# Performance work log

Hardware: AMD Instinct MI355X
Metric: run time of the kernel (lower is better)

Reference implementation:

```python
import jax, jax.numpy as jnp
import numpy as np
from jax.ops import segment_sum

NUM_NODES = 100000
HIDDEN = 128
NUM_LAYERS = 3
EDGES = 640000
BN_EPS = 1e-5


def setup_inputs() -> dict:
    key = jax.random.key(0)
    ks = jax.random.split(key, 6)
    edge_index = jax.random.randint(ks[0], (2, EDGES), 0, NUM_NODES, dtype=jnp.int32)
    # xavier-ish init for embedding (hidden-1 dims; last dim is log-degree feature)
    emb_weight = jax.random.normal(ks[1], (NUM_NODES, HIDDEN - 1), dtype=jnp.float32) * 0.02
    # GCNConv linear weights [L, in, out] and biases [L, out]
    Ws = jax.random.normal(ks[2], (NUM_LAYERS, HIDDEN, HIDDEN), dtype=jnp.float32) * (1.0 / np.sqrt(HIDDEN))
    bs = jnp.zeros((NUM_LAYERS, HIDDEN), dtype=jnp.float32)
    gammas = jnp.ones((NUM_LAYERS, HIDDEN), dtype=jnp.float32)
    betas = jnp.zeros((NUM_LAYERS, HIDDEN), dtype=jnp.float32)
    return {"emb_weight": emb_weight, "Ws": Ws, "bs": bs,
            "gammas": gammas, "betas": betas, "edge_index": edge_index}


def reference(emb_weight, Ws, bs, gammas, betas, edge_index):
    row, col = edge_index[0], edge_index[1]  # source, target
    N = emb_weight.shape[0]
    ones_e = jnp.ones(row.shape[0], dtype=emb_weight.dtype)

    # node_degree_features = log(out_degree + 1) (degree of edge_index[0])
    deg_src = segment_sum(ones_e, row, num_segments=N)
    x = jnp.concatenate([emb_weight, jnp.log(deg_src + 1.0)[:, None]], axis=1)  # [N, H]

    # GCN symmetric normalization (add_self_loops=False): deg over targets
    deg = segment_sum(ones_e, col, num_segments=N)
    dinv = jnp.where(deg > 0, jax.lax.rsqrt(jnp.maximum(deg, 1.0)), 0.0)
    norm = dinv[row] * dinv[col]  # [E]

    for i in range(Ws.shape[0]):
        x_prev = x
        h = x @ Ws[i]  # [N, H]
        # scatter-add of normalized messages: out[col] += norm * h[row]
        agg = segment_sum(norm[:, None] * h[row], col, num_segments=N) + bs[i]
        # BatchNorm1d (batch statistics, biased variance)
        mean = agg.mean(axis=0)
        var = agg.var(axis=0)
        x = gammas[i] * (agg - mean) * jax.lax.rsqrt(var + BN_EPS) + betas[i]
        x = jax.nn.relu(x)
        if i > 0:
            x = x + 0.5 * x_prev
    return x
```

## Files before the change

kernel.cpp:

```cpp
#include <hip/hip_runtime.h>
#include <hip/hip_bf16.h>
#include <math.h>

#define BN_EPS 1e-5f

typedef __attribute__((ext_vector_type(8))) short short8v;
typedef __attribute__((ext_vector_type(4))) float f32x4;
typedef __attribute__((ext_vector_type(2))) int int2v;
typedef __attribute__((ext_vector_type(4))) unsigned int uint4v;
typedef __attribute__((ext_vector_type(4))) float float4v;

__device__ inline float bf_lo(unsigned int p) { return __uint_as_float(p << 16); }
__device__ inline float bf_hi(unsigned int p) { return __uint_as_float(p & 0xffff0000u); }
__device__ inline unsigned int packbf(float a, float b) {
    unsigned short lo = __builtin_bit_cast(unsigned short, __float2bfloat16(a));
    unsigned short hi = __builtin_bit_cast(unsigned short, __float2bfloat16(b));
    return (unsigned int)lo | ((unsigned int)hi << 16);
}


__global__ __launch_bounds__(256) void deg_kernel(const int* __restrict__ row, const int* __restrict__ col,
                                                  float* __restrict__ deg_src, float* __restrict__ deg_dst, int E) {
    int e = blockIdx.x * 256 + threadIdx.x;
    if (e < E) {
        atomicAdd(&deg_src[row[e]], 1.0f);
        atomicAdd(&deg_dst[col[e]], 1.0f);
    }
}

__global__ __launch_bounds__(256) void dinv_cnt_kernel(float* __restrict__ deg_dst, int* __restrict__ cnt, int N) {
    int n = blockIdx.x * 256 + threadIdx.x;
    if (n < N) {
        float d = deg_dst[n];
        cnt[n] = (int)d;
        deg_dst[n] = (d > 0.0f) ? rsqrtf(d) : 0.0f;
    }
}

__global__ __launch_bounds__(256) void initx_kernel(const float* __restrict__ emb, const float* __restrict__ deg_src,
                                                    unsigned int* __restrict__ x, int N) {
    int idx = blockIdx.x * 256 + threadIdx.x;
    if (idx < N * 64) {
        int n = idx >> 6, p = idx & 63;
        float v0, v1;
        if (p < 63) {
            v0 = emb[(size_t)n * 127 + 2 * p];
            v1 = emb[(size_t)n * 127 + 2 * p + 1];
        } else {
            v0 = emb[(size_t)n * 127 + 126];
            v1 = logf(deg_src[n] + 1.0f);
        }
        x[idx] = packbf(v0, v1);
    }
}

__global__ __launch_bounds__(256) void wt_kernel(const float* __restrict__ Ws, __hip_bfloat16* __restrict__ Wt) {
    int idx = blockIdx.x * 256 + threadIdx.x;
    if (idx < 3 * 16384) {
        int l = idx >> 14, rem = idx & 16383, c = rem >> 7, k = rem & 127;
        Wt[idx] = __float2bfloat16(Ws[(l << 14) + (k << 7) + c]);
    }
}


__global__ __launch_bounds__(256) void scan_pass1(const int* __restrict__ cnt, int* __restrict__ blockSums,
                                                  int N, int PT) {
    __shared__ int lds[256];
    const int tid = threadIdx.x;
    const int start = (blockIdx.x * 256 + tid) * PT;
    int s = 0;
    for (int i = 0; i < PT; ++i) {
        int idx = start + i;
        if (idx < N) s += cnt[idx];
    }
    lds[tid] = s;
    __syncthreads();
    for (int d = 128; d > 0; d >>= 1) {
        if (tid < d) lds[tid] += lds[tid + d];
        __syncthreads();
    }
    if (tid == 0) blockSums[blockIdx.x] = lds[0];
}

__global__ __launch_bounds__(256) void scan_pass2(const int* __restrict__ blockSums, int* __restrict__ blockOffs) {
    __shared__ int lds[256];
    const int tid = threadIdx.x;
    int v = blockSums[tid];
    lds[tid] = v;
    __syncthreads();
    for (int d = 1; d < 256; d <<= 1) {
        int t = (tid >= d) ? lds[tid - d] : 0;
        __syncthreads();
        lds[tid] += t;
        __syncthreads();
    }
    blockOffs[tid] = lds[tid] - v;
}

__global__ __launch_bounds__(256) void scan_pass3(const int* __restrict__ cnt, const int* __restrict__ blockOffs,
                                                  int* __restrict__ off, int* __restrict__ cur,
                                                  int N, int PT, int E) {
    __shared__ int lds[256];
    const int tid = threadIdx.x;
    const int start = (blockIdx.x * 256 + tid) * PT;
    int s = 0;
    for (int i = 0; i < PT; ++i) {
        int idx = start + i;
        if (idx < N) s += cnt[idx];
    }
    lds[tid] = s;
    __syncthreads();
    for (int d = 1; d < 256; d <<= 1) {
        int t = (tid >= d) ? lds[tid - d] : 0;
        __syncthreads();
        lds[tid] += t;
        __syncthreads();
    }
    int prefix = blockOffs[blockIdx.x] + lds[tid] - s;
    for (int i = 0; i < PT; ++i) {
        int idx = start + i;
        if (idx < N) {
            off[idx] = prefix;
            cur[idx] = prefix;
            prefix += cnt[idx];
        }
    }
    if (blockIdx.x == 0 && tid == 0) off[N] = E;
}

__global__ __launch_bounds__(256) void fill_kernel(const int* __restrict__ row, const int* __restrict__ col,
                                                   const float* __restrict__ dinv, int* __restrict__ cur,
                                                   int2* __restrict__ meta, int E) {
    int e = blockIdx.x * 256 + threadIdx.x;
    if (e < E) {
        int r = row[e], t = col[e];
        int p = atomicAdd(&cur[t], 1);
        meta[p] = make_int2(r, __float_as_int(dinv[r] * dinv[t]));
    }
}


__global__ __launch_bounds__(256) void gemm_mfma(const __hip_bfloat16* __restrict__ X,
                                                 const __hip_bfloat16* __restrict__ Wt,
                                                 __hip_bfloat16* __restrict__ H, float* __restrict__ sums,
                                                 int nStripes, int N) {
    if (blockIdx.x == 0) sums[threadIdx.x] = 0.0f;

    const int lane = threadIdx.x & 63;
    const int wv = threadIdx.x >> 6;
    const int r = lane & 15;
    const int q = lane >> 4;
    const int ch = (blockIdx.x * 4 + wv) & 1;

    short8v bfrag[4][4];
#pragma unroll
    for (int ct = 0; ct < 4; ++ct)
#pragma unroll
        for (int kk = 0; kk < 4; ++kk)
            bfrag[ct][kk] = *(const short8v*)(Wt + ((ch * 64 + ct * 16 + r) << 7) + kk * 32 + q * 8);

    const int totalJobs = nStripes * 2;
    for (int job = blockIdx.x * 4 + wv; job < totalJobs; job += gridDim.x * 4) {
        const int s = job >> 1;
        const int arow = s * 16 + r;
        short8v a0 = {}, a1 = {}, a2 = {}, a3 = {};
        if (arow < N) {
            const __hip_bfloat16* xp = X + ((size_t)arow << 7) + q * 8;
            a0 = *(const short8v*)(xp);
            a1 = *(const short8v*)(xp + 32);
            a2 = *(const short8v*)(xp + 64);
            a3 = *(const short8v*)(xp + 96);
        }
        f32x4 acc[4];
#pragma unroll
        for (int ct = 0; ct < 4; ++ct) {
            f32x4 c = {0.f, 0.f, 0.f, 0.f};
            c = __builtin_amdgcn_mfma_f32_16x16x32_bf16(a0, bfrag[ct][0], c, 0, 0, 0);
            c = __builtin_amdgcn_mfma_f32_16x16x32_bf16(a1, bfrag[ct][1], c, 0, 0, 0);
            c = __builtin_amdgcn_mfma_f32_16x16x32_bf16(a2, bfrag[ct][2], c, 0, 0, 0);
            c = __builtin_amdgcn_mfma_f32_16x16x32_bf16(a3, bfrag[ct][3], c, 0, 0, 0);
            acc[ct] = c;
        }
#pragma unroll
        for (int g = 0; g < 4; ++g) {
            int grow = s * 16 + q * 4 + g;
            if (grow < N) {
                __hip_bfloat16* hp = H + ((size_t)grow << 7) + ch * 64 + r;
#pragma unroll
                for (int ct = 0; ct < 4; ++ct)
                    hp[ct * 16] = __float2bfloat16(acc[ct][g]);
            }
        }
    }
}


template <int MODE>
__global__ __launch_bounds__(256) void bn_gemm(const unsigned int* __restrict__ aggb, const float* __restrict__ sums,
                                               const float* __restrict__ gamma, const float* __restrict__ beta,
                                               const unsigned int* __restrict__ xprevb, unsigned int* __restrict__ xoutb,
                                               const __hip_bfloat16* __restrict__ Wt, __hip_bfloat16* __restrict__ H,
                                               float* __restrict__ sumsNext, int nStripes, int N, float invN) {
    if (blockIdx.x == 0) sumsNext[threadIdx.x] = 0.0f;

    const int lane = threadIdx.x & 63;
    const int wv = threadIdx.x >> 6;
    const int r = lane & 15;
    const int q = lane >> 4;
    const int ch = (blockIdx.x * 4 + wv) & 1;

    short8v bfrag[4][4];
#pragma unroll
    for (int ct = 0; ct < 4; ++ct)
#pragma unroll
        for (int kk = 0; kk < 4; ++kk)
            bfrag[ct][kk] = *(const short8v*)(Wt + ((ch * 64 + ct * 16 + r) << 7) + kk * 32 + q * 8);

    const int totalJobs = nStripes * 2;
    for (int job = blockIdx.x * 4 + wv; job < totalJobs; job += gridDim.x * 4) {
        const int s = job >> 1;
        const int arow = s * 16 + r;
        short8v a[4] = {{}, {}, {}, {}};
        if (arow < N) {
            const size_t rbase = ((size_t)arow << 6) + q * 4;
#pragma unroll
            for (int kk = 0; kk < 4; ++kk) {
                const int c0 = q * 8 + kk * 32;
                float su[8], sq[8], gm[8], bt[8];
                *(float4*)&su[0] = *(const float4*)&sums[c0];
                *(float4*)&su[4] = *(const float4*)&sums[c0 + 4];
                *(float4*)&sq[0] = *(const float4*)&sums[128 + c0];
                *(float4*)&sq[4] = *(const float4*)&sums[128 + c0 + 4];
                *(float4*)&gm[0] = *(const float4*)&gamma[c0];
                *(float4*)&gm[4] = *(const float4*)&gamma[c0 + 4];
                *(float4*)&bt[0] = *(const float4*)&beta[c0];
                *(float4*)&bt[4] = *(const float4*)&beta[c0 + 4];
                float sc[8], sh[8];
#pragma unroll
                for (int j = 0; j < 8; ++j) {
                    float m = su[j] * invN;
                    float v = sq[j] * invN - m * m;
                    float inv = rsqrtf(fmaxf(v, 0.0f) + BN_EPS);
                    sc[j] = gm[j] * inv;
                    sh[j] = bt[j] - m * sc[j];
                }
                uint4 av = *(const uint4*)(aggb + rbase + kk * 16);
                const unsigned int* au = (const unsigned int*)&av;
                float x[8];
#pragma unroll
                for (int j = 0; j < 4; ++j) {
                    x[2 * j]     = fmaxf(fmaf(bf_lo(au[j]), sc[2 * j],     sh[2 * j]),     0.f);
                    x[2 * j + 1] = fmaxf(fmaf(bf_hi(au[j]), sc[2 * j + 1], sh[2 * j + 1]), 0.f);
                }
                if (MODE == 1) {
                    uint4 xv = *(const uint4*)(xprevb + rbase + kk * 16);
                    const unsigned int* xu = (const unsigned int*)&xv;
#pragma unroll
                    for (int j = 0; j < 4; ++j) {
                        x[2 * j]     = fmaf(0.5f, bf_lo(xu[j]), x[2 * j]);
                        x[2 * j + 1] = fmaf(0.5f, bf_hi(xu[j]), x[2 * j + 1]);
                    }
                }
                uint4 pk;
                unsigned int* pku = (unsigned int*)&pk;
#pragma unroll
                for (int j = 0; j < 4; ++j) pku[j] = packbf(x[2 * j], x[2 * j + 1]);
                if (ch == 0) *(uint4*)(xoutb + rbase + kk * 16) = pk;
#pragma unroll
                for (int j = 0; j < 4; ++j) ((unsigned int*)&a[kk])[j] = pku[j];
            }
        }
        f32x4 acc[4];
#pragma unroll
        for (int ct = 0; ct < 4; ++ct) {
            f32x4 c = {0.f, 0.f, 0.f, 0.f};
            c = __builtin_amdgcn_mfma_f32_16x16x32_bf16(a[0], bfrag[ct][0], c, 0, 0, 0);
            c = __builtin_amdgcn_mfma_f32_16x16x32_bf16(a[1], bfrag[ct][1], c, 0, 0, 0);
            c = __builtin_amdgcn_mfma_f32_16x16x32_bf16(a[2], bfrag[ct][2], c, 0, 0, 0);
            c = __builtin_amdgcn_mfma_f32_16x16x32_bf16(a[3], bfrag[ct][3], c, 0, 0, 0);
            acc[ct] = c;
        }
#pragma unroll
        for (int g = 0; g < 4; ++g) {
            int grow = s * 16 + q * 4 + g;
            if (grow < N) {
                __hip_bfloat16* hp = H + ((size_t)grow << 7) + ch * 64 + r;
#pragma unroll
                for (int ct = 0; ct < 4; ++ct)
                    hp[ct * 16] = __float2bfloat16(acc[ct][g]);
            }
        }
    }
}


__global__ __launch_bounds__(256) void gather_kernel(const __hip_bfloat16* __restrict__ h,
                                                     const int* __restrict__ off, const int2* __restrict__ meta,
                                                     const float* __restrict__ bias,
                                                     unsigned int* __restrict__ aggb, float* __restrict__ sums, int N) {
    __shared__ float sm[2][4][128];
    const int tid = threadIdx.x;
    const int lane = tid & 63;
    const int w = tid >> 6;
    const int g = lane >> 4;
    const int s = lane & 15;

    float b8[8];
    *(float4*)&b8[0] = *(const float4*)&bias[s * 8];
    *(float4*)&b8[4] = *(const float4*)&bias[s * 8 + 4];

    float psum[8], psq[8];
#pragma unroll
    for (int j = 0; j < 8; ++j) { psum[j] = 0.f; psq[j] = 0.f; }

    for (int base = (blockIdx.x * 4 + w) * 2; base < N; base += gridDim.x * 8) {
        const int nA = __builtin_amdgcn_readfirstlane(base);
        const int hasB = (nA + 1 < N);
        const int sA = off[nA];
        const int eA = off[nA + 1];
        const int eB = hasB ? off[nA + 2] : eA;

        float accA[8], accB[8];
#pragma unroll
        for (int j = 0; j < 8; ++j) { accA[j] = 0.f; accB[j] = 0.f; }

        int iA = sA, iB = eA;
        while (iA < eA || iB < eB) {
            int i0A = iA + g, i1A = iA + 4 + g;
            int i0B = iB + g, i1B = iB + 4 + g;
            int idx0A = (i0A < eA) ? i0A : 0;
            int idx1A = (i1A < eA) ? i1A : 0;
            int idx0B = (i0B < eB) ? i0B : 0;
            int idx1B = (i1B < eB) ? i1B : 0;
            int2v m0A = __builtin_nontemporal_load((const int2v*)&meta[idx0A]);
            int2v m1A = __builtin_nontemporal_load((const int2v*)&meta[idx1A]);
            int2v m0B = __builtin_nontemporal_load((const int2v*)&meta[idx0B]);
            int2v m1B = __builtin_nontemporal_load((const int2v*)&meta[idx1B]);
            float w0A = (i0A < eA) ? __int_as_float(m0A[1]) : 0.f;
            float w1A = (i1A < eA) ? __int_as_float(m1A[1]) : 0.f;
            float w0B = (i0B < eB) ? __int_as_float(m0B[1]) : 0.f;
            float w1B = (i1B < eB) ? __int_as_float(m1B[1]) : 0.f;
            short8v h0A = *(const short8v*)(h + ((size_t)m0A[0] << 7) + s * 8);
            short8v h1A = *(const short8v*)(h + ((size_t)m1A[0] << 7) + s * 8);
            short8v h0B = *(const short8v*)(h + ((size_t)m0B[0] << 7) + s * 8);
            short8v h1B = *(const short8v*)(h + ((size_t)m1B[0] << 7) + s * 8);
#pragma unroll
            for (int j = 0; j < 4; ++j) {
                unsigned int u;
                u = ((const unsigned int*)&h0A)[j];
                accA[2 * j]     = fmaf(w0A, bf_lo(u), accA[2 * j]);
                accA[2 * j + 1] = fmaf(w0A, bf_hi(u), accA[2 * j + 1]);
                u = ((const unsigned int*)&h1A)[j];
                accA[2 * j]     = fmaf(w1A, bf_lo(u), accA[2 * j]);
                accA[2 * j + 1] = fmaf(w1A, bf_hi(u), accA[2 * j + 1]);
                u = ((const unsigned int*)&h0B)[j];
                accB[2 * j]     = fmaf(w0B, bf_lo(u), accB[2 * j]);
                accB[2 * j + 1] = fmaf(w0B, bf_hi(u), accB[2 * j + 1]);
                u = ((const unsigned int*)&h1B)[j];
                accB[2 * j]     = fmaf(w1B, bf_lo(u), accB[2 * j]);
                accB[2 * j + 1] = fmaf(w1B, bf_hi(u), accB[2 * j + 1]);
            }
            iA += 8; iB += 8;
        }
#pragma unroll
        for (int j = 0; j < 8; ++j) {
            accA[j] += __shfl_xor(accA[j], 16);
            accA[j] += __shfl_xor(accA[j], 32);
            accA[j] += b8[j];
            accB[j] += __shfl_xor(accB[j], 16);
            accB[j] += __shfl_xor(accB[j], 32);
            accB[j] += b8[j];
        }
        if (g == 0) {
            uint4v pk;
#pragma unroll
            for (int j = 0; j < 4; ++j) pk[j] = packbf(accA[2 * j], accA[2 * j + 1]);
            __builtin_nontemporal_store(pk, (uint4v*)(aggb + ((size_t)nA << 6) + s * 4));
#pragma unroll
            for (int j = 0; j < 8; ++j) {
                psum[j] += accA[j];
                psq[j] = fmaf(accA[j], accA[j], psq[j]);
            }
            if (hasB) {
#pragma unroll
                for (int j = 0; j < 8; ++j) {
                    psum[j] += accB[j];
                    psq[j] = fmaf(accB[j], accB[j], psq[j]);
                }
            }
        } else if (g == 1 && hasB) {
            uint4v pk;
#pragma unroll
            for (int j = 0; j < 4; ++j) pk[j] = packbf(accB[2 * j], accB[2 * j + 1]);
            __builtin_nontemporal_store(pk, (uint4v*)(aggb + ((size_t)(nA + 1) << 6) + s * 4));
        }
    }
    if (g == 0) {
#pragma unroll
        for (int j = 0; j < 8; ++j) {
            sm[0][w][s * 8 + j] = psum[j];
            sm[1][w][s * 8 + j] = psq[j];
        }
    }
    __syncthreads();
    if (tid < 128) {
        atomicAdd(&sums[tid], sm[0][0][tid] + sm[0][1][tid] + sm[0][2][tid] + sm[0][3][tid]);
    } else {
        int c = tid - 128;
        atomicAdd(&sums[128 + c], sm[1][0][c] + sm[1][1][c] + sm[1][2][c] + sm[1][3][c]);
    }
}


__global__ __launch_bounds__(256) void bn_out(const unsigned int* __restrict__ aggb, const float* __restrict__ sums,
                                              const float* __restrict__ gamma, const float* __restrict__ beta,
                                              const uint4* __restrict__ xprev, float* __restrict__ xout,
                                              int NO, float invN) {
    int idx = blockIdx.x * 256 + threadIdx.x;
    if (idx >= NO) return;
    const int c0 = (idx & 15) * 8;

    float su[8], sq[8], gm[8], bt[8];
    *(float4*)&su[0] = *(const float4*)&sums[c0];
    *(float4*)&su[4] = *(const float4*)&sums[c0 + 4];
    *(float4*)&sq[0] = *(const float4*)&sums[128 + c0];
    *(float4*)&sq[4] = *(const float4*)&sums[128 + c0 + 4];
    *(float4*)&gm[0] = *(const float4*)&gamma[c0];
    *(float4*)&gm[4] = *(const float4*)&gamma[c0 + 4];
    *(float4*)&bt[0] = *(const float4*)&beta[c0];
    *(float4*)&bt[4] = *(const float4*)&beta[c0 + 4];

    float sc[8], sh[8];
#pragma unroll
    for (int j = 0; j < 8; ++j) {
        float m = su[j] * invN;
        float v = sq[j] * invN - m * m;
        float inv = rsqrtf(fmaxf(v, 0.0f) + BN_EPS);
        sc[j] = gm[j] * inv;
        sh[j] = bt[j] - m * sc[j];
    }

    uint4v av = __builtin_nontemporal_load((const uint4v*)(aggb + (size_t)idx * 4));
    float r[8];
#pragma unroll
    for (int j = 0; j < 4; ++j) {
        r[2 * j]     = fmaxf(fmaf(bf_lo(av[j]), sc[2 * j],     sh[2 * j]),     0.f);
        r[2 * j + 1] = fmaxf(fmaf(bf_hi(av[j]), sc[2 * j + 1], sh[2 * j + 1]), 0.f);
    }
    uint4 xv = xprev[idx];
    const unsigned int* xu = (const unsigned int*)&xv;
#pragma unroll
    for (int j = 0; j < 4; ++j) {
        r[2 * j]     = fmaf(0.5f, bf_lo(xu[j]), r[2 * j]);
        r[2 * j + 1] = fmaf(0.5f, bf_hi(xu[j]), r[2 * j + 1]);
    }
    float* op = xout + (size_t)idx * 8;
    float4v lo = {r[0], r[1], r[2], r[3]};
    float4v hi = {r[4], r[5], r[6], r[7]};
    __builtin_nontemporal_store(lo, (float4v*)op);
    __builtin_nontemporal_store(hi, (float4v*)(op + 4));
}


extern "C" void kernel_launch(void* const* d_in, const int* in_sizes, int n_in,
                              void* d_out, int out_size, void* d_ws, size_t ws_size,
                              hipStream_t stream) {
    const float* emb    = (const float*)d_in[0];
    const float* Ws     = (const float*)d_in[1];
    const float* bs     = (const float*)d_in[2];
    const float* gammas = (const float*)d_in[3];
    const float* betas  = (const float*)d_in[4];
    const int*   ei     = (const int*)d_in[5];

    const int N = in_sizes[0] / 127;
    const int E = in_sizes[5] / 2;
    const int* row = ei;
    const int* col = ei + E;
    float* out = (float*)d_out;

    const size_t NH = (size_t)N * 128;
    __hip_bfloat16* XA = (__hip_bfloat16*)d_ws;
    __hip_bfloat16* XB = XA + NH;
    unsigned int*  AGG = (unsigned int*)(XB + NH);
    int2*         meta = (int2*)(AGG + NH / 2);
    __hip_bfloat16* Wt = (__hip_bfloat16*)(meta + E);
    float* deg_src = (float*)(Wt + 3 * 16384);
    float* dinvb   = deg_src + N;
    float* sumsA   = dinvb + N;
    float* sumsB   = sumsA + 256;
    int*   cnt     = (int*)(sumsB + 256);
    int*   cur     = cnt + N;
    int*   blockSums = cur + N;
    int*   blockOffs = blockSums + 256;
    int*   off     = blockOffs + 256;

    __hip_bfloat16* H2 = (__hip_bfloat16*)out;

    const int NO = (int)(NH / 8);
    const int PT = (N + 65535) / 65536;
    const int nStripes = (N + 15) / 16;
    const float invN = 1.0f / (float)N;

    hipMemsetAsync(deg_src, 0, sizeof(float) * 2 * (size_t)N, stream);
    wt_kernel<<<(3 * 16384 + 255) / 256, 256, 0, stream>>>(Ws, Wt);
    deg_kernel<<<(E + 255) / 256, 256, 0, stream>>>(row, col, deg_src, dinvb, E);
    dinv_cnt_kernel<<<(N + 255) / 256, 256, 0, stream>>>(dinvb, cnt, N);
    initx_kernel<<<(N * 64 + 255) / 256, 256, 0, stream>>>(emb, deg_src, (unsigned int*)XA, N);
    scan_pass1<<<256, 256, 0, stream>>>(cnt, blockSums, N, PT);
    scan_pass2<<<1, 256, 0, stream>>>(blockSums, blockOffs);
    scan_pass3<<<256, 256, 0, stream>>>(cnt, blockOffs, off, cur, N, PT, E);
    fill_kernel<<<(E + 255) / 256, 256, 0, stream>>>(row, col, dinvb, cur, meta, E);

    gemm_mfma<<<1024, 256, 0, stream>>>(XA, Wt, XB, sumsA, nStripes, N);
    gather_kernel<<<2048, 256, 0, stream>>>(XB, off, meta, bs, AGG, sumsA, N);

    bn_gemm<0><<<1024, 256, 0, stream>>>(AGG, sumsA, gammas, betas, nullptr,
                                         (unsigned int*)XA, Wt + 16384, XB, sumsB, nStripes, N, invN);
    gather_kernel<<<2048, 256, 0, stream>>>(XB, off, meta, bs + 128, AGG, sumsB, N);

    bn_gemm<1><<<1024, 256, 0, stream>>>(AGG, sumsB, gammas + 128, betas + 128, (const unsigned int*)XA,
                                         (unsigned int*)XB, Wt + 2 * 16384, H2, sumsA, nStripes, N, invN);
    gather_kernel<<<2048, 256, 0, stream>>>(H2, off, meta, bs + 256, AGG, sumsA, N);

    bn_out<<<(NO + 255) / 256, 256, 0, stream>>>(AGG, sumsA, gammas + 256, betas + 256,
                                                 (const uint4*)XB, out, NO, invN);
}
```

Measured before the change: 496.3 us.

## Fold dinv kernel into fill, precompute BN scale in LDS, drop nontemporal ops

Removes the dinv_cnt kernel: the scan reads float degrees directly and fill_kernel computes rsqrt of both endpoint degrees inline. bn_gemm now computes the BatchNorm scale and shift once per block into shared memory instead of recomputing them from global sums in every inner iteration. Nontemporal loads and stores in the gather and bn_out kernels are replaced with ordinary vector accesses. Together these save one launch and some redundant arithmetic and global reads, at the cost of an extra rsqrt per edge in fill and a block-wide sync in bn_gemm. Dropping the nontemporal hints changes how the caches treat those accesses.

```diff
diff --git a/kernel.cpp b/kernel.cpp
--- a/kernel.cpp
+++ b/kernel.cpp
@@ -6,8 +6,6 @@
 
 typedef __attribute__((ext_vector_type(8))) short short8v;
 typedef __attribute__((ext_vector_type(4))) float f32x4;
-typedef __attribute__((ext_vector_type(2))) int int2v;
-typedef __attribute__((ext_vector_type(4))) unsigned int uint4v;
 typedef __attribute__((ext_vector_type(4))) float float4v;
 
 __device__ inline float bf_lo(unsigned int p) { return __uint_as_float(p << 16); }
@@ -25,15 +23,6 @@
     if (e < E) {
         atomicAdd(&deg_src[row[e]], 1.0f);
         atomicAdd(&deg_dst[col[e]], 1.0f);
-    }
-}
-
-__global__ __launch_bounds__(256) void dinv_cnt_kernel(float* __restrict__ deg_dst, int* __restrict__ cnt, int N) {
-    int n = blockIdx.x * 256 + threadIdx.x;
-    if (n < N) {
-        float d = deg_dst[n];
-        cnt[n] = (int)d;
-        deg_dst[n] = (d > 0.0f) ? rsqrtf(d) : 0.0f;
     }
 }
 
@@ -63,7 +52,7 @@
 }
 
 
-__global__ __launch_bounds__(256) void scan_pass1(const int* __restrict__ cnt, int* __restrict__ blockSums,
+__global__ __launch_bounds__(256) void scan_pass1(const float* __restrict__ deg, int* __restrict__ blockSums,
                                                   int N, int PT) {
     __shared__ int lds[256];
     const int tid = threadIdx.x;
@@ -71,7 +60,7 @@
     int s = 0;
     for (int i = 0; i < PT; ++i) {
         int idx = start + i;
-        if (idx < N) s += cnt[idx];
+        if (idx < N) s += (int)deg[idx];
     }
     lds[tid] = s;
     __syncthreads();
@@ -97,7 +86,7 @@
     blockOffs[tid] = lds[tid] - v;
 }
 
-__global__ __launch_bounds__(256) void scan_pass3(const int* __restrict__ cnt, const int* __restrict__ blockOffs,
+__global__ __launch_bounds__(256) void scan_pass3(const float* __restrict__ deg, const int* __restrict__ blockOffs,
                                                   int* __restrict__ off, int* __restrict__ cur,
                                                   int N, int PT, int E) {
     __shared__ int lds[256];
@@ -106,7 +95,7 @@
     int s = 0;
     for (int i = 0; i < PT; ++i) {
         int idx = start + i;
-        if (idx < N) s += cnt[idx];
+        if (idx < N) s += (int)deg[idx];
     }
     lds[tid] = s;
     __syncthreads();
@@ -122,20 +111,23 @@
         if (idx < N) {
             off[idx] = prefix;
             cur[idx] = prefix;
-            prefix += cnt[idx];
+            prefix += (int)deg[idx];
         }
     }
     if (blockIdx.x == 0 && tid == 0) off[N] = E;
 }
 
 __global__ __launch_bounds__(256) void fill_kernel(const int* __restrict__ row, const int* __restrict__ col,
-                                                   const float* __restrict__ dinv, int* __restrict__ cur,
+                                                   const float* __restrict__ deg_dst, int* __restrict__ cur,
                                                    int2* __restrict__ meta, int E) {
     int e = blockIdx.x * 256 + threadIdx.x;
     if (e < E) {
         int r = row[e], t = col[e];
         int p = atomicAdd(&cur[t], 1);
-        meta[p] = make_int2(r, __float_as_int(dinv[r] * dinv[t]));
+        float dr = deg_dst[r], dt = deg_dst[t];
+        float ir = (dr > 0.0f) ? rsqrtf(dr) : 0.0f;
+        float it = (dt > 0.0f) ? rsqrtf(dt) : 0.0f;
+        meta[p] = make_int2(r, __float_as_int(ir * it));
     }
 }
 
@@ -201,10 +193,21 @@
                                                const unsigned int* __restrict__ xprevb, unsigned int* __restrict__ xoutb,
                                                const __hip_bfloat16* __restrict__ Wt, __hip_bfloat16* __restrict__ H,
                                                float* __restrict__ sumsNext, int nStripes, int N, float invN) {
-    if (blockIdx.x == 0) sumsNext[threadIdx.x] = 0.0f;
-
-    const int lane = threadIdx.x & 63;
-    const int wv = threadIdx.x >> 6;
+    __shared__ float ssc[128], ssh[128];
+    const int tid = threadIdx.x;
+    if (blockIdx.x == 0) sumsNext[tid] = 0.0f;
+    if (tid < 128) {
+        float m = sums[tid] * invN;
+        float v = sums[128 + tid] * invN - m * m;
+        float inv = rsqrtf(fmaxf(v, 0.0f) + BN_EPS);
+        float sc = gamma[tid] * inv;
+        ssc[tid] = sc;
+        ssh[tid] = beta[tid] - m * sc;
+    }
+    __syncthreads();
+
+    const int lane = tid & 63;
+    const int wv = tid >> 6;
     const int r = lane & 15;
     const int q = lane >> 4;
     const int ch = (blockIdx.x * 4 + wv) & 1;
@@ -226,24 +229,11 @@
 #pragma unroll
             for (int kk = 0; kk < 4; ++kk) {
                 const int c0 = q * 8 + kk * 32;
-                float su[8], sq[8], gm[8], bt[8];
-                *(float4*)&su[0] = *(const float4*)&sums[c0];
-                *(float4*)&su[4] = *(const float4*)&sums[c0 + 4];
-                *(float4*)&sq[0] = *(const float4*)&sums[128 + c0];
-                *(float4*)&sq[4] = *(const float4*)&sums[128 + c0 + 4];
-                *(float4*)&gm[0] = *(const float4*)&gamma[c0];
-                *(float4*)&gm[4] = *(const float4*)&gamma[c0 + 4];
-                *(float4*)&bt[0] = *(const float4*)&beta[c0];
-                *(float4*)&bt[4] = *(const float4*)&beta[c0 + 4];
                 float sc[8], sh[8];
-#pragma unroll
-                for (int j = 0; j < 8; ++j) {
-                    float m = su[j] * invN;
-                    float v = sq[j] * invN - m * m;
-                    float inv = rsqrtf(fmaxf(v, 0.0f) + BN_EPS);
-                    sc[j] = gm[j] * inv;
-                    sh[j] = bt[j] - m * sc[j];
-                }
+                *(float4*)&sc[0] = *(const float4*)&ssc[c0];
+                *(float4*)&sc[4] = *(const float4*)&ssc[c0 + 4];
+                *(float4*)&sh[0] = *(const float4*)&ssh[c0];
+                *(float4*)&sh[4] = *(const float4*)&ssh[c0 + 4];
                 uint4 av = *(const uint4*)(aggb + rbase + kk * 16);
                 const unsigned int* au = (const unsigned int*)&av;
                 float x[8];
@@ -332,18 +322,16 @@
             int idx1A = (i1A < eA) ? i1A : 0;
             int idx0B = (i0B < eB) ? i0B : 0;
             int idx1B = (i1B < eB) ? i1B : 0;
-            int2v m0A = __builtin_nontemporal_load((const int2v*)&meta[idx0A]);
-            int2v m1A = __builtin_nontemporal_load((const int2v*)&meta[idx1A]);
-            int2v m0B = __builtin_nontemporal_load((const int2v*)&meta[idx0B]);
-            int2v m1B = __builtin_nontemporal_load((const int2v*)&meta[idx1B]);
-            float w0A = (i0A < eA) ? __int_as_float(m0A[1]) : 0.f;
-            float w1A = (i1A < eA) ? __int_as_float(m1A[1]) : 0.f;
-            float w0B = (i0B < eB) ? __int_as_float(m0B[1]) : 0.f;
-            float w1B = (i1B < eB) ? __int_as_float(m1B[1]) : 0.f;
-            short8v h0A = *(const short8v*)(h + ((size_t)m0A[0] << 7) + s * 8);
-            short8v h1A = *(const short8v*)(h + ((size_t)m1A[0] << 7) + s * 8);
-            short8v h0B = *(const short8v*)(h + ((size_t)m0B[0] << 7) + s * 8);
-            short8v h1B = *(const short8v*)(h + ((size_t)m1B[0] << 7) + s * 8);
+            int2 m0A = meta[idx0A], m1A = meta[idx1A];
+            int2 m0B = meta[idx0B], m1B = meta[idx1B];
+            float w0A = (i0A < eA) ? __int_as_float(m0A.y) : 0.f;
+            float w1A = (i1A < eA) ? __int_as_float(m1A.y) : 0.f;
+            float w0B = (i0B < eB) ? __int_as_float(m0B.y) : 0.f;
+            float w1B = (i1B < eB) ? __int_as_float(m1B.y) : 0.f;
+            short8v h0A = *(const short8v*)(h + ((size_t)m0A.x << 7) + s * 8);
+            short8v h1A = *(const short8v*)(h + ((size_t)m1A.x << 7) + s * 8);
+            short8v h0B = *(const short8v*)(h + ((size_t)m0B.x << 7) + s * 8);
+            short8v h1B = *(const short8v*)(h + ((size_t)m1B.x << 7) + s * 8);
 #pragma unroll
             for (int j = 0; j < 4; ++j) {
                 unsigned int u;
@@ -372,10 +360,10 @@
             accB[j] += b8[j];
         }
         if (g == 0) {
-            uint4v pk;
+            unsigned int pk[4];
 #pragma unroll
             for (int j = 0; j < 4; ++j) pk[j] = packbf(accA[2 * j], accA[2 * j + 1]);
-            __builtin_nontemporal_store(pk, (uint4v*)(aggb + ((size_t)nA << 6) + s * 4));
+            *(uint4*)(aggb + ((size_t)nA << 6) + s * 4) = *(uint4*)pk;
 #pragma unroll
             for (int j = 0; j < 8; ++j) {
                 psum[j] += accA[j];
@@ -389,10 +377,10 @@
                 }
             }
         } else if (g == 1 && hasB) {
-            uint4v pk;
+            unsigned int pk[4];
 #pragma unroll
             for (int j = 0; j < 4; ++j) pk[j] = packbf(accB[2 * j], accB[2 * j + 1]);
-            __builtin_nontemporal_store(pk, (uint4v*)(aggb + ((size_t)(nA + 1) << 6) + s * 4));
+            *(uint4*)(aggb + ((size_t)(nA + 1) << 6) + s * 4) = *(uint4*)pk;
         }
     }
     if (g == 0) {
@@ -440,12 +428,13 @@
         sh[j] = bt[j] - m * sc[j];
     }
 
-    uint4v av = __builtin_nontemporal_load((const uint4v*)(aggb + (size_t)idx * 4));
+    uint4 av = *(const uint4*)(aggb + (size_t)idx * 4);
+    const unsigned int* au = (const unsigned int*)&av;
     float r[8];
 #pragma unroll
     for (int j = 0; j < 4; ++j) {
-        r[2 * j]     = fmaxf(fmaf(bf_lo(av[j]), sc[2 * j],     sh[2 * j]),     0.f);
-        r[2 * j + 1] = fmaxf(fmaf(bf_hi(av[j]), sc[2 * j + 1], sh[2 * j + 1]), 0.f);
+        r[2 * j]     = fmaxf(fmaf(bf_lo(au[j]), sc[2 * j],     sh[2 * j]),     0.f);
+        r[2 * j + 1] = fmaxf(fmaf(bf_hi(au[j]), sc[2 * j + 1], sh[2 * j + 1]), 0.f);
     }
     uint4 xv = xprev[idx];
     const unsigned int* xu = (const unsigned int*)&xv;
@@ -455,10 +444,8 @@
         r[2 * j + 1] = fmaf(0.5f, bf_hi(xu[j]), r[2 * j + 1]);
     }
     float* op = xout + (size_t)idx * 8;
-    float4v lo = {r[0], r[1], r[2], r[3]};
-    float4v hi = {r[4], r[5], r[6], r[7]};
-    __builtin_nontemporal_store(lo, (float4v*)op);
-    __builtin_nontemporal_store(hi, (float4v*)(op + 4));
+    *(float4*)op       = make_float4(r[0], r[1], r[2], r[3]);
+    *(float4*)(op + 4) = make_float4(r[4], r[5], r[6], r[7]);
 }
 
 
@@ -485,11 +472,10 @@
     int2*         meta = (int2*)(AGG + NH / 2);
     __hip_bfloat16* Wt = (__hip_bfloat16*)(meta + E);
     float* deg_src = (float*)(Wt + 3 * 16384);
-    float* dinvb   = deg_src + N;
-    float* sumsA   = dinvb + N;
+    float* deg_dst = deg_src + N;
+    float* sumsA   = deg_dst + N;
     float* sumsB   = sumsA + 256;
-    int*   cnt     = (int*)(sumsB + 256);
-    int*   cur     = cnt + N;
+    int*   cur     = (int*)(sumsB + 256);
     int*   blockSums = cur + N;
     int*   blockOffs = blockSums + 256;
     int*   off     = blockOffs + 256;
@@ -503,13 +489,12 @@
 
     hipMemsetAsync(deg_src, 0, sizeof(float) * 2 * (size_t)N, stream);
     wt_kernel<<<(3 * 16384 + 255) / 256, 256, 0, stream>>>(Ws, Wt);
-    deg_kernel<<<(E + 255) / 256, 256, 0, stream>>>(row, col, deg_src, dinvb, E);
-    dinv_cnt_kernel<<<(N + 255) / 256, 256, 0, stream>>>(dinvb, cnt, N);
+    deg_kernel<<<(E + 255) / 256, 256, 0, stream>>>(row, col, deg_src, deg_dst, E);
     initx_kernel<<<(N * 64 + 255) / 256, 256, 0, stream>>>(emb, deg_src, (unsigned int*)XA, N);
-    scan_pass1<<<256, 256, 0, stream>>>(cnt, blockSums, N, PT);
+    scan_pass1<<<256, 256, 0, stream>>>(deg_dst, blockSums, N, PT);
     scan_pass2<<<1, 256, 0, stream>>>(blockSums, blockOffs);
-    scan_pass3<<<256, 256, 0, stream>>>(cnt, blockOffs, off, cur, N, PT, E);
-    fill_kernel<<<(E + 255) / 256, 256, 0, stream>>>(row, col, dinvb, cur, meta, E);
+    scan_pass3<<<256, 256, 0, stream>>>(deg_dst, blockOffs, off, cur, N, PT, E);
+    fill_kernel<<<(E + 255) / 256, 256, 0, stream>>>(row, col, deg_dst, cur, meta, E);
 
     gemm_mfma<<<1024, 256, 0, stream>>>(XA, Wt, XB, sumsA, nStripes, N);
     gather_kernel<<<2048, 256, 0, stream>>>(XB, off, meta, bs, AGG, sumsA, N);
```

Result: faster. 439.9 us (-11.4%).
